# Kernel tuning notes

Hardware: AMD Instinct MI355X
Metric: run time of the kernel (lower is better)

Reference implementation:

```python
import jax, jax.numpy as jnp
import numpy as np

S, B, D, H = 2048, 2, 1024, 16
DK = D // H
SCALE = 1.0 / np.sqrt(DK)


def setup_inputs() -> dict:
    key = jax.random.key(0)
    ks = jax.random.split(key, 8)
    return {
        "query": jax.random.normal(ks[0], (S, B, D), dtype=jnp.float32),
        "key": jax.random.normal(ks[1], (S, B, D), dtype=jnp.float32),
        "value": jax.random.normal(ks[2], (S, B, D), dtype=jnp.float32),
        "mask": jax.random.randint(ks[3], (B, S, S), 0, 2, dtype=jnp.int32),
        "in_proj_weight": jax.random.normal(ks[4], (3 * D, D), dtype=jnp.float32) * 0.02,
        "in_proj_bias": jax.random.normal(ks[5], (3 * D,), dtype=jnp.float32) * 0.02,
        "out_proj_weight": jax.random.normal(ks[6], (D, D), dtype=jnp.float32) * 0.02,
        "out_proj_bias": jax.random.normal(ks[7], (D,), dtype=jnp.float32) * 0.02,
    }


def reference(query, key, value, mask, in_proj_weight, in_proj_bias,
              out_proj_weight, out_proj_bias):
    seq_len, batch, d_model = query.shape
    # split fused in-projection: order is query, key, value
    Wq, Wk, Wv = in_proj_weight[:D], in_proj_weight[D:2 * D], in_proj_weight[2 * D:]
    bq, bk, bv = in_proj_bias[:D], in_proj_bias[D:2 * D], in_proj_bias[2 * D:]
    # PrepareForMultiHeadAttention: x @ W^T + b, then split heads -> [s, b, h, d_k]
    q = (query @ Wq.T + bq).reshape(seq_len, batch, H, DK)
    k = (key @ Wk.T + bk).reshape(key.shape[0], batch, H, DK)
    v = (value @ Wv.T + bv).reshape(value.shape[0], batch, H, DK)
    # scores [i, j, b, h] in float32, scaled
    scores = jnp.einsum('ibhd,jbhd->ijbh', q, k).astype(jnp.float32) * SCALE
    # mask: [b, q, k] -> permute(1,2,0) -> [q, k, b] -> unsqueeze(-1)
    m = jnp.transpose(mask, (1, 2, 0))[..., None]
    scores = jnp.where(m == 1, jnp.float32(-1e9), scores)
    # softmax over key axis (dim=1)
    attn = jax.nn.softmax(scores, axis=1)
    # dropout p=0.0 -> identity
    x = jnp.einsum('ijbh,jbhd->ibhd', attn, v).reshape(seq_len, batch, -1)
    return x @ out_proj_weight.T + out_proj_bias
```

## Files before the change

kernel.cpp:

```cpp
#include <hip/hip_runtime.h>
#include <hip/hip_bf16.h>

typedef unsigned short u16;
typedef unsigned int   u32;
typedef unsigned long long u64;
typedef __bf16 bf16x8 __attribute__((ext_vector_type(8)));
typedef float  f32x4  __attribute__((ext_vector_type(4)));

#define S_LEN  2048
#define BATCH  2
#define DMODEL 1024
#define NHEADS 16
#define DKH    64
#define MWORDS (S_LEN/64)
#define ATT_SCALE 0.125f

__device__ __forceinline__ u16 f2bf(float f){
  u32 x = __builtin_bit_cast(u32, f);
  x += 0x7fffu + ((x >> 16) & 1u);
  return (u16)(x >> 16);
}
__device__ __forceinline__ bf16x8 ld8(const u16* p){ return *(const bf16x8*)p; }

__device__ __forceinline__ void gload16(const u16* g, u16* l){
  __builtin_amdgcn_global_load_lds(
      (const __attribute__((address_space(1))) u32*)(u64)g,
      (__attribute__((address_space(3))) u32*)(u64)l,
      16, 0, 0);
}

__global__ __launch_bounds__(256) void cvt_kernel(
    const float* __restrict__ a0, const float* __restrict__ a1, const float* __restrict__ a2,
    const float* __restrict__ wi, const float* __restrict__ wo, const int* __restrict__ msk,
    u16* __restrict__ d0, u16* __restrict__ d1, u16* __restrict__ d2,
    u16* __restrict__ dwi, u16* __restrict__ dwo, u64* __restrict__ mbits)
{
  int tid = blockIdx.x*256 + threadIdx.x;
  int stride = gridDim.x*256;
  const int NX = S_LEN*BATCH*DMODEL/4;
  for (int i = tid; i < NX; i += stride){
    f32x4 x0 = ((const f32x4*)a0)[i];
    f32x4 x1 = ((const f32x4*)a1)[i];
    f32x4 x2 = ((const f32x4*)a2)[i];
    ((ushort4*)d0)[i] = make_ushort4(f2bf(x0[0]), f2bf(x0[1]), f2bf(x0[2]), f2bf(x0[3]));
    ((ushort4*)d1)[i] = make_ushort4(f2bf(x1[0]), f2bf(x1[1]), f2bf(x1[2]), f2bf(x1[3]));
    ((ushort4*)d2)[i] = make_ushort4(f2bf(x2[0]), f2bf(x2[1]), f2bf(x2[2]), f2bf(x2[3]));
  }
  const int NWI = 3*DMODEL*DMODEL/4;
  for (int i = tid; i < NWI; i += stride){
    f32x4 x = ((const f32x4*)wi)[i];
    ((ushort4*)dwi)[i] = make_ushort4(f2bf(x[0]), f2bf(x[1]), f2bf(x[2]), f2bf(x[3]));
  }
  const int NWO = DMODEL*DMODEL/4;
  for (int i = tid; i < NWO; i += stride){
    f32x4 x = ((const f32x4*)wo)[i];
    ((ushort4*)dwo)[i] = make_ushort4(f2bf(x[0]), f2bf(x[1]), f2bf(x[2]), f2bf(x[3]));
  }
  int gw   = tid >> 6;
  int lane = threadIdx.x & 63;
  int nwaves = stride >> 6;
  const int NW = BATCH*S_LEN*MWORDS;
  for (int w = gw; w < NW; w += nwaves){
    int v = msk[(size_t)w*64 + lane];
    u64 bits = __ballot(v != 0);
    if (lane == 0) mbits[w] = bits;
  }
}

__device__ __forceinline__ void gemm128_loop(
    const u16* __restrict__ A, const u16* __restrict__ W,
    u16* abuf, u16* bbuf, int tid, f32x4 acc[4][4])
{
  int lane = tid & 63, quad = lane >> 4, r = lane & 15;
  int wv = tid >> 6, wm = (wv & 1)*64, wn = (wv >> 1)*64;
  int c0 = tid, c1 = tid + 256;
  int r0 = c0 >> 2, g0 = ((c0 & 3) ^ (r0 & 3))*8;
  int r1 = c1 >> 2, g1 = ((c1 & 3) ^ (r1 & 3))*8;
  const u16* ga0 = A + (size_t)r0*DMODEL + g0;
  const u16* ga1 = A + (size_t)r1*DMODEL + g1;
  const u16* gb0 = W + (size_t)r0*DMODEL + g0;
  const u16* gb1 = W + (size_t)r1*DMODEL + g1;
  u16* la0 = abuf + c0*8;  u16* la1 = abuf + c1*8;
  u16* lb0 = bbuf + c0*8;  u16* lb1 = bbuf + c1*8;
  int sw = (quad ^ (r & 3))*8;

  for (int k0 = 0; k0 < DMODEL; k0 += 32){
    __syncthreads();
    gload16(ga0 + k0, la0);
    gload16(ga1 + k0, la1);
    gload16(gb0 + k0, lb0);
    gload16(gb1 + k0, lb1);
    __syncthreads();
    bf16x8 af[4], bfr[4];
    #pragma unroll
    for (int i = 0; i < 4; ++i) af[i]  = ld8(&abuf[(wm + i*16 + r)*32 + sw]);
    #pragma unroll
    for (int i = 0; i < 4; ++i) bfr[i] = ld8(&bbuf[(wn + i*16 + r)*32 + sw]);
    #pragma unroll
    for (int mi = 0; mi < 4; ++mi)
      #pragma unroll
      for (int ni = 0; ni < 4; ++ni)
        acc[mi][ni] = __builtin_amdgcn_mfma_f32_16x16x32_bf16(af[mi], bfr[ni], acc[mi][ni], 0,0,0);
  }
}

__global__ __launch_bounds__(256) void qkv_proj_kernel(
    const u16* __restrict__ xq, const u16* __restrict__ xk, const u16* __restrict__ xv,
    const u16* __restrict__ w, const float* __restrict__ bias,
    u16* __restrict__ q_ws, u16* __restrict__ k_ws, u16* __restrict__ vt_ws)
{
  __shared__ __align__(16) u16 abuf[128*32];
  __shared__ __align__(16) u16 bbuf[128*32];
  int tid = threadIdx.x;
  int lane = tid & 63, quad = lane >> 4, r = lane & 15;
  int wv = tid >> 6, wm = (wv & 1)*64, wn = (wv >> 1)*64;
  int m0 = blockIdx.x*128, n0 = blockIdx.y*128;
  int t = n0 >> 10;
  const u16* X = (t == 0) ? xq : (t == 1) ? xk : xv;

  f32x4 acc[4][4] = {};
  gemm128_loop(X + (size_t)m0*DMODEL, w + (size_t)n0*DMODEL, abuf, bbuf, tid, acc);

  int mbase = m0 + wm, nbase = n0 + wn;
  #pragma unroll
  for (int ni = 0; ni < 4; ++ni){
    int n  = nbase + ni*16 + r;
    float bv = bias[n];
    int nn = n & (DMODEL-1);
    int h = nn >> 6, dk = nn & 63;
    #pragma unroll
    for (int mi = 0; mi < 4; ++mi){
      #pragma unroll
      for (int reg = 0; reg < 4; ++reg){
        int m = mbase + mi*16 + quad*4 + reg;
        int s = m >> 1, b = m & 1;
        u16 hv = f2bf(acc[mi][ni][reg] + bv);
        size_t bh = (size_t)(b*NHEADS + h);
        if (t == 0)      q_ws [(bh*S_LEN + s)*DKH + dk] = hv;
        else if (t == 1) k_ws [(bh*S_LEN + s)*DKH + dk] = hv;
        else             vt_ws[(bh*DKH + dk)*S_LEN + s] = hv;
      }
    }
  }
}

__global__ __launch_bounds__(256) void attn_kernel(
    const u16* __restrict__ q_ws, const u16* __restrict__ k_ws, const u16* __restrict__ vt_ws,
    const u64* __restrict__ mbits, u16* __restrict__ x_ws)
{
  __shared__ __align__(16) u16 kbuf[64*72];
  __shared__ __align__(16) u16 vbuf[64*72];
  __shared__ __align__(16) u16 pbuf[4][16*72];
  int tid  = threadIdx.x;
  int wv   = tid >> 6;
  int lane = tid & 63;
  int quad = lane >> 4, r = lane & 15;
  int bh = blockIdx.y;
  int b  = bh >> 4, h = bh & 15;
  int i0 = (blockIdx.x*4 + wv) * 16;

  const u16* Q  = q_ws  + (size_t)bh*S_LEN*DKH;
  const u16* K  = k_ws  + (size_t)bh*S_LEN*DKH;
  const u16* Vt = vt_ws + (size_t)bh*DKH*S_LEN;
  const u64* MB = mbits + ((size_t)b*S_LEN + (i0 + r))*MWORDS;

  int f1 = tid + 256;
  int sr0 = tid >> 3, sc0 = (tid & 7)*8;
  int sr1 = f1  >> 3, sc1 = (f1  & 7)*8;

  const u16* qrow = Q + (size_t)(i0 + r)*DKH + quad*8;
  bf16x8 qf0 = ld8(qrow), qf1 = ld8(qrow + 32);

  float l_part = 0.f;
  f32x4 o[4] = {};
  f32x4 z = {0.f, 0.f, 0.f, 0.f};
  u16* pl = pbuf[wv];

  for (int j0 = 0; j0 < S_LEN; j0 += 64){
    u64 mb = MB[j0 >> 6];
    __syncthreads();
    *(bf16x8*)&kbuf[sr0*72 + sc0] = ld8(K  + (size_t)(j0 + sr0)*DKH  + sc0);
    *(bf16x8*)&kbuf[sr1*72 + sc1] = ld8(K  + (size_t)(j0 + sr1)*DKH  + sc1);
    *(bf16x8*)&vbuf[sr0*72 + sc0] = ld8(Vt + (size_t)sr0*S_LEN + j0 + sc0);
    *(bf16x8*)&vbuf[sr1*72 + sc1] = ld8(Vt + (size_t)sr1*S_LEN + j0 + sc1);
    __syncthreads();

    float p[16];
    #pragma unroll
    for (int c = 0; c < 4; ++c){
      bf16x8 ka = ld8(&kbuf[(16*c + r)*72 + quad*8]);
      bf16x8 kb = ld8(&kbuf[(16*c + r)*72 + 32 + quad*8]);
      f32x4 s = __builtin_amdgcn_mfma_f32_16x16x32_bf16(ka, qf0, z, 0,0,0);
      s       = __builtin_amdgcn_mfma_f32_16x16x32_bf16(kb, qf1, s, 0,0,0);
      u32 mc = (u32)(mb >> (16*c + 4*quad));
      p[c*4+0] = (mc & 1u) ? 0.f : __expf(s[0]*ATT_SCALE);
      p[c*4+1] = (mc & 2u) ? 0.f : __expf(s[1]*ATT_SCALE);
      p[c*4+2] = (mc & 4u) ? 0.f : __expf(s[2]*ATT_SCALE);
      p[c*4+3] = (mc & 8u) ? 0.f : __expf(s[3]*ATT_SCALE);
      l_part += p[c*4+0] + p[c*4+1] + p[c*4+2] + p[c*4+3];
    }
    #pragma unroll
    for (int c = 0; c < 4; ++c)
      *(ushort4*)&pl[r*72 + 16*c + quad*4] =
        make_ushort4(f2bf(p[c*4+0]), f2bf(p[c*4+1]), f2bf(p[c*4+2]), f2bf(p[c*4+3]));
    asm volatile("s_waitcnt lgkmcnt(0)" ::: "memory");
    bf16x8 pf0 = ld8(&pl[r*72 + quad*8]);
    bf16x8 pf1 = ld8(&pl[r*72 + 32 + quad*8]);
    #pragma unroll
    for (int tt = 0; tt < 4; ++tt){
      bf16x8 va = ld8(&vbuf[(tt*16 + r)*72 + quad*8]);
      bf16x8 vb = ld8(&vbuf[(tt*16 + r)*72 + 32 + quad*8]);
      o[tt] = __builtin_amdgcn_mfma_f32_16x16x32_bf16(pf0, va, o[tt], 0,0,0);
      o[tt] = __builtin_amdgcn_mfma_f32_16x16x32_bf16(pf1, vb, o[tt], 0,0,0);
    }
  }

  l_part += __shfl_xor(l_part, 16, 64);
  l_part += __shfl_xor(l_part, 32, 64);
  float l0 = 1.f/__shfl(l_part, quad*4+0, 64);
  float l1 = 1.f/__shfl(l_part, quad*4+1, 64);
  float l2 = 1.f/__shfl(l_part, quad*4+2, 64);
  float l3 = 1.f/__shfl(l_part, quad*4+3, 64);
  #pragma unroll
  for (int tt = 0; tt < 4; ++tt){
    int col = h*DKH + tt*16 + r;
    x_ws[((size_t)(i0 + quad*4 + 0)*BATCH + b)*DMODEL + col] = f2bf(o[tt][0]*l0);
    x_ws[((size_t)(i0 + quad*4 + 1)*BATCH + b)*DMODEL + col] = f2bf(o[tt][1]*l1);
    x_ws[((size_t)(i0 + quad*4 + 2)*BATCH + b)*DMODEL + col] = f2bf(o[tt][2]*l2);
    x_ws[((size_t)(i0 + quad*4 + 3)*BATCH + b)*DMODEL + col] = f2bf(o[tt][3]*l3);
  }
}

__global__ __launch_bounds__(256) void out_proj_kernel(
    const u16* __restrict__ x, const u16* __restrict__ w, const float* __restrict__ bias,
    float* __restrict__ out)
{
  __shared__ __align__(16) u16 abuf[128*32];
  __shared__ __align__(16) u16 bbuf[128*32];
  int tid = threadIdx.x;
  int lane = tid & 63, quad = lane >> 4, r = lane & 15;
  int wv = tid >> 6, wm = (wv & 1)*64, wn = (wv >> 1)*64;
  int m0 = blockIdx.x*128, n0 = blockIdx.y*128;

  f32x4 acc[4][4] = {};
  gemm128_loop(x + (size_t)m0*DMODEL, w + (size_t)n0*DMODEL, abuf, bbuf, tid, acc);

  int mbase = m0 + wm, nbase = n0 + wn;
  #pragma unroll
  for (int ni = 0; ni < 4; ++ni){
    int n = nbase + ni*16 + r;
    float bv = bias[n];
    #pragma unroll
    for (int mi = 0; mi < 4; ++mi){
      #pragma unroll
      for (int reg = 0; reg < 4; ++reg){
        int m = mbase + mi*16 + quad*4 + reg;
        out[(size_t)m*DMODEL + n] = acc[mi][ni][reg] + bv;
      }
    }
  }
}

extern "C" void kernel_launch(void* const* d_in, const int* in_sizes, int n_in,
                              void* d_out, int out_size, void* d_ws, size_t ws_size,
                              hipStream_t stream) {
  (void)in_sizes; (void)n_in; (void)out_size; (void)ws_size;
  const float* query = (const float*)d_in[0];
  const float* key   = (const float*)d_in[1];
  const float* value = (const float*)d_in[2];
  const int*   mask  = (const int*)d_in[3];
  const float* w_in  = (const float*)d_in[4];
  const float* b_in  = (const float*)d_in[5];
  const float* w_out = (const float*)d_in[6];
  const float* b_out = (const float*)d_in[7];
  float* out = (float*)d_out;

  const size_t TSZ = (size_t)BATCH*NHEADS*S_LEN*DKH;
  const size_t XSZ = (size_t)S_LEN*BATCH*DMODEL;
  u16* q_ws  = (u16*)d_ws;
  u16* k_ws  = q_ws  + TSZ;
  u16* vt_ws = k_ws  + TSZ;
  u16* x_ws  = vt_ws + TSZ;
  u16* xq_bf = x_ws  + XSZ;
  u16* xk_bf = xq_bf + XSZ;
  u16* xv_bf = xk_bf + XSZ;
  u16* wi_bf = xv_bf + XSZ;
  u16* wo_bf = wi_bf + (size_t)3*DMODEL*DMODEL;
  u64* mb_ws = (u64*)(wo_bf + (size_t)DMODEL*DMODEL);

  cvt_kernel<<<1024, 256, 0, stream>>>(query, key, value, w_in, w_out, mask,
                                       xq_bf, xk_bf, xv_bf, wi_bf, wo_bf, mb_ws);
  qkv_proj_kernel<<<dim3(32, 24), 256, 0, stream>>>(xq_bf, xk_bf, xv_bf, wi_bf, b_in,
                                                    q_ws, k_ws, vt_ws);
  attn_kernel<<<dim3(32, 32), 256, 0, stream>>>(q_ws, k_ws, vt_ws, mb_ws, x_ws);
  out_proj_kernel<<<dim3(32, 8), 256, 0, stream>>>(x_ws, wo_bf, b_out, out);
}
```

Baseline: 287.4 us.

## Stage K/V tiles via direct global-to-LDS loads in fragment order, use exp2

K and V tiles are now copied straight from global memory into LDS with global_load_lds. They are stored in a permuted, MFMA-fragment-ordered layout, so each lane reads its operand with one contiguous 16-byte LDS load, with no padding and no register staging. The softmax exponent switches from __expf to the hardware exp2 with the scale folded into one constant. The bf16 packing of probabilities uses a cheaper round-half-up plus byte permute in place of round-to-nearest-even. The risks are a missing vmcnt wait before the barrier, which could let reads see incomplete LDS data, and a slight change in bf16 rounding.

Result: no change. 289.3 us (+0.7%).

```diff
diff --git a/kernel.cpp b/kernel.cpp
--- a/kernel.cpp
+++ b/kernel.cpp
@@ -14,6 +14,7 @@
 #define DKH    64
 #define MWORDS (S_LEN/64)
 #define ATT_SCALE 0.125f
+#define C2EXP 0.18033688011112f
 
 __device__ __forceinline__ u16 f2bf(float f){
   u32 x = __builtin_bit_cast(u32, f);
@@ -148,8 +149,8 @@
     const u16* __restrict__ q_ws, const u16* __restrict__ k_ws, const u16* __restrict__ vt_ws,
     const u64* __restrict__ mbits, u16* __restrict__ x_ws)
 {
-  __shared__ __align__(16) u16 kbuf[64*72];
-  __shared__ __align__(16) u16 vbuf[64*72];
+  __shared__ __align__(16) u16 kperm[64*64];
+  __shared__ __align__(16) u16 vperm[64*64];
   __shared__ __align__(16) u16 pbuf[4][16*72];
   int tid  = threadIdx.x;
   int wv   = tid >> 6;
@@ -164,9 +165,12 @@
   const u16* Vt = vt_ws + (size_t)bh*DKH*S_LEN;
   const u64* MB = mbits + ((size_t)b*S_LEN + (i0 + r))*MWORDS;
 
-  int f1 = tid + 256;
-  int sr0 = tid >> 3, sc0 = (tid & 7)*8;
-  int sr1 = f1  >> 3, sc1 = (f1  & 7)*8;
+  const u16* gk0 = K  + (size_t)(16*wv + r)*DKH + quad*8;
+  const u16* gk1 = gk0 + 32;
+  const u16* gv0 = Vt + (size_t)(16*wv + r)*S_LEN + quad*8;
+  const u16* gv1 = gv0 + 32;
+  u16* lk = kperm + (size_t)wv*128*8;
+  u16* lv = vperm + (size_t)wv*128*8;
 
   const u16* qrow = Q + (size_t)(i0 + r)*DKH + quad*8;
   bf16x8 qf0 = ld8(qrow), qf1 = ld8(qrow + 32);
@@ -179,37 +183,43 @@
   for (int j0 = 0; j0 < S_LEN; j0 += 64){
     u64 mb = MB[j0 >> 6];
     __syncthreads();
-    *(bf16x8*)&kbuf[sr0*72 + sc0] = ld8(K  + (size_t)(j0 + sr0)*DKH  + sc0);
-    *(bf16x8*)&kbuf[sr1*72 + sc1] = ld8(K  + (size_t)(j0 + sr1)*DKH  + sc1);
-    *(bf16x8*)&vbuf[sr0*72 + sc0] = ld8(Vt + (size_t)sr0*S_LEN + j0 + sc0);
-    *(bf16x8*)&vbuf[sr1*72 + sc1] = ld8(Vt + (size_t)sr1*S_LEN + j0 + sc1);
+    gload16(gk0, lk);  gload16(gk1, lk + 512);
+    gload16(gv0, lv);  gload16(gv1, lv + 512);
+    gk0 += 64*DKH; gk1 += 64*DKH; gv0 += 64; gv1 += 64;
     __syncthreads();
 
     float p[16];
     #pragma unroll
     for (int c = 0; c < 4; ++c){
-      bf16x8 ka = ld8(&kbuf[(16*c + r)*72 + quad*8]);
-      bf16x8 kb = ld8(&kbuf[(16*c + r)*72 + 32 + quad*8]);
+      bf16x8 ka = ld8(&kperm[(2*c + 0)*512 + lane*8]);
+      bf16x8 kb = ld8(&kperm[(2*c + 1)*512 + lane*8]);
       f32x4 s = __builtin_amdgcn_mfma_f32_16x16x32_bf16(ka, qf0, z, 0,0,0);
       s       = __builtin_amdgcn_mfma_f32_16x16x32_bf16(kb, qf1, s, 0,0,0);
       u32 mc = (u32)(mb >> (16*c + 4*quad));
-      p[c*4+0] = (mc & 1u) ? 0.f : __expf(s[0]*ATT_SCALE);
-      p[c*4+1] = (mc & 2u) ? 0.f : __expf(s[1]*ATT_SCALE);
-      p[c*4+2] = (mc & 4u) ? 0.f : __expf(s[2]*ATT_SCALE);
-      p[c*4+3] = (mc & 8u) ? 0.f : __expf(s[3]*ATT_SCALE);
+      p[c*4+0] = (mc & 1u) ? 0.f : __builtin_amdgcn_exp2f(s[0]*C2EXP);
+      p[c*4+1] = (mc & 2u) ? 0.f : __builtin_amdgcn_exp2f(s[1]*C2EXP);
+      p[c*4+2] = (mc & 4u) ? 0.f : __builtin_amdgcn_exp2f(s[2]*C2EXP);
+      p[c*4+3] = (mc & 8u) ? 0.f : __builtin_amdgcn_exp2f(s[3]*C2EXP);
       l_part += p[c*4+0] + p[c*4+1] + p[c*4+2] + p[c*4+3];
     }
     #pragma unroll
-    for (int c = 0; c < 4; ++c)
-      *(ushort4*)&pl[r*72 + 16*c + quad*4] =
-        make_ushort4(f2bf(p[c*4+0]), f2bf(p[c*4+1]), f2bf(p[c*4+2]), f2bf(p[c*4+3]));
+    for (int c = 0; c < 4; ++c){
+      u32 e0 = __builtin_bit_cast(u32, p[c*4+0]) + 0x8000u;
+      u32 o0 = __builtin_bit_cast(u32, p[c*4+1]) + 0x8000u;
+      u32 e1 = __builtin_bit_cast(u32, p[c*4+2]) + 0x8000u;
+      u32 o1 = __builtin_bit_cast(u32, p[c*4+3]) + 0x8000u;
+      uint2 pk;
+      pk.x = __builtin_amdgcn_perm(o0, e0, 0x07060302u);
+      pk.y = __builtin_amdgcn_perm(o1, e1, 0x07060302u);
+      *(uint2*)&pl[r*72 + 16*c + quad*4] = pk;
+    }
     asm volatile("s_waitcnt lgkmcnt(0)" ::: "memory");
     bf16x8 pf0 = ld8(&pl[r*72 + quad*8]);
     bf16x8 pf1 = ld8(&pl[r*72 + 32 + quad*8]);
     #pragma unroll
     for (int tt = 0; tt < 4; ++tt){
-      bf16x8 va = ld8(&vbuf[(tt*16 + r)*72 + quad*8]);
-      bf16x8 vb = ld8(&vbuf[(tt*16 + r)*72 + 32 + quad*8]);
+      bf16x8 va = ld8(&vperm[(2*tt + 0)*512 + lane*8]);
+      bf16x8 vb = ld8(&vperm[(2*tt + 1)*512 + lane*8]);
       o[tt] = __builtin_amdgcn_mfma_f32_16x16x32_bf16(pf0, va, o[tt], 0,0,0);
       o[tt] = __builtin_amdgcn_mfma_f32_16x16x32_bf16(pf1, vb, o[tt], 0,0,0);
     }
```
